# Kernel optimization log

Hardware: AMD Instinct MI355X
Metric: run time of the kernel (lower is better)

The kernel has to match this reference:

```python
import jax, jax.numpy as jnp
import numpy as np

N = 4096
D = 512
NC_RATIO = 0.1
GAMMA = 0.8
REG = 0.03
NITER = 100
THRESH = 1e-4


def setup_inputs() -> dict:
    key = jax.random.key(0)
    k1, k2, k3 = jax.random.split(key, 3)

    def unit(k):
        x = jax.random.normal(k, (N, D), dtype=jnp.float32)
        return x / jnp.linalg.norm(x, axis=1, keepdims=True)

    return {
        "image_embeds": unit(k1),
        "text_embeds": unit(k2),
        "text_no_embeds": unit(k3),
        "logit_scale": jnp.ones((), dtype=jnp.float32),
    }


def _sinkhorn_log(p, q, C, mask):
    """Log-domain Sinkhorn, faithful to sinkhorn_log_domain_torch (incl. early stop)."""
    logp, logq = jnp.log(p), jnp.log(q)

    def Mfun(u, v):
        Mm = (-C + u[:, None] + v[None, :]) / REG
        return jnp.where(mask == 0, jnp.float32(-1e6), Mm)

    def lse(A):  # log-sum-exp over axis 1, with the original +1e-10
        mx = jnp.max(A, axis=1, keepdims=True)
        return jnp.log(jnp.sum(jnp.exp(A - mx), axis=1) + 1e-10) + mx[:, 0]

    def cond(s):
        i, u, v, err = s
        return jnp.logical_and(i < NITER, err >= THRESH)

    def body(s):
        i, u, v, _ = s
        u1 = u
        u = REG * (logp - lse(Mfun(u, v))) + u
        v = REG * (logq - lse(Mfun(u, v).T)) + v
        return i + 1, u, v, jnp.sum(jnp.abs(u - u1))

    _, u, v, _ = jax.lax.while_loop(
        cond, body, (jnp.int32(0), 0.0 * p, 0.0 * q, jnp.float32(jnp.inf))
    )
    return jnp.exp(Mfun(u, v))


def _kl_batchmean(log_probs, target):
    # torch KLDivLoss(reduction='batchmean'): sum(t*(log t - lp)) / batch, t=0 -> 0
    pointwise = jnp.where(target > 0, target * jnp.log(target), 0.0) - target * log_probs
    return jnp.sum(pointwise) / target.shape[0]


def _forward(image_embeds, text_embeds, text_no_embeds, logit_scale):
    n = image_embeds.shape[0]
    scale = jnp.exp(logit_scale)
    sims = image_embeds @ text_embeds.T                        # [N, N]
    sims_no = jnp.sum(image_embeds * text_no_embeds, axis=1)[:, None]  # [N, 1]
    logits = jnp.concatenate([scale * sims, scale * sims_no], axis=1)  # [N, N+1]

    # ---- torch.no_grad() label construction ----
    sims_sg = jax.lax.stop_gradient(sims)
    sims_no_sg = jax.lax.stop_gradient(sims_no)
    scale_sg = jax.lax.stop_gradient(scale)

    # infoNCE_preds with temp = 1/scale
    pos = jnp.exp(jnp.diag(sims_sg) * scale_sg)
    neg_sum = jnp.sum(jnp.exp(sims_sg * scale_sg), axis=1) - pos
    preds = pos / (pos + neg_sum)
    nc_num = int(NC_RATIO * n)
    _, nc_ids = jax.lax.top_k(-preds, nc_num)  # smallest preds

    S = jnp.concatenate([sims_sg, sims_no_sg], axis=1)  # [N, N+1]
    cost_v = 1.0 - S
    cost_v = cost_v / jnp.max(cost_v)
    cost_t = 1.0 - S.T
    cost_t = cost_t / jnp.max(cost_t)
    p = jnp.full((n,), 1.0 / n, dtype=jnp.float32)
    q = jnp.full((n + 1,), 1.0 / (n + 1), dtype=jnp.float32)

    Mv = (jnp.ones((n, n + 1), dtype=jnp.int32)
          .at[:, -1].set(0)
          .at[nc_ids, nc_ids].set(0)
          .at[nc_ids, -1].set(1))

    pi_v = _sinkhorn_log(p, q, cost_v, Mv)
    pi_t = _sinkhorn_log(q, p, cost_t, Mv.T)

    idx = jnp.arange(n)
    Lv = (jnp.zeros((n, n + 1), dtype=jnp.float32)
          .at[idx, idx].set(1.0)
          .at[nc_ids, nc_ids].set(0.0)
          .at[nc_ids, -1].set(1.0))

    label_v2t = GAMMA * (pi_v / jnp.sum(pi_v, axis=1, keepdims=True)) + (1.0 - GAMMA) * Lv
    label_t2v = GAMMA * (pi_t / jnp.sum(pi_t, axis=1, keepdims=True)) + (1.0 - GAMMA) * Lv.T
    label_v2t = jax.lax.stop_gradient(label_v2t)
    label_t2v = jax.lax.stop_gradient(label_t2v)
    # ---- end no_grad ----

    loss_img = _kl_batchmean(jax.nn.log_softmax(logits, axis=1), label_v2t)
    loss_txt = _kl_batchmean(jax.nn.log_softmax(logits.T, axis=1), label_t2v)
    loss_ul = (loss_img + loss_txt) / 2.0

    cos = jnp.sum(text_embeds * text_no_embeds, axis=1)
    loss_op = jnp.mean(jnp.maximum(cos + 0.2, 0.0) + jnp.maximum(-0.7 - cos, 0.0))
    return loss_ul, loss_op


def reference(image_embeds, text_embeds, text_no_embeds, logit_scale):
    return _forward(image_embeds, text_embeds, text_no_embeds, logit_scale)
```

## Files before the change

kernel.cpp:

```cpp
#include <hip/hip_runtime.h>
#include <hip/hip_bf16.h>


#define NN 4096
#define LDA 4104
#define DD 512
#define NCNUM 409
#define REGc 0.03f
#define INVREG (1.0f/0.03f)
#define GAM 0.8f
#define THRESHc 1e-4f
#define LOGN 8.3177661667193433f
#define LOGM 8.3180102775477533f
#define NEGINF (-__builtin_inff())

typedef unsigned short u16;
typedef unsigned int u32;
typedef _Float16 f16;

struct alignas(16) Q  { u32 x, y, z, w; };
union H8 { Q q; f16 h[8]; };

typedef __attribute__((ext_vector_type(8))) short frag_ab;
typedef __attribute__((ext_vector_type(4))) float frag_cd;

__device__ __forceinline__ float bf2f(u32 u) { return __uint_as_float(u << 16); }
__device__ __forceinline__ float bflo(u32 w) { return __uint_as_float(w << 16); }
__device__ __forceinline__ float bfhi(u32 w) { return __uint_as_float(w & 0xFFFF0000u); }
__device__ __forceinline__ u16 f2bf_rne(float f) {
  u32 b = __float_as_uint(f);
  b += 0x7FFFu + ((b >> 16) & 1u);
  return (u16)(b >> 16);
}
__device__ __forceinline__ u16 f2h_hw(float f) {
  union { f16 h; u16 u; } X; X.h = (f16)f; return X.u;
}
__device__ __forceinline__ float h2f_hw(u16 v) {
  union { u16 u; f16 h; } X; X.u = v; return (float)X.h;
}
__device__ __forceinline__ float exp2_fast(float x) {
#if __has_builtin(__builtin_amdgcn_exp2f)
  return __builtin_amdgcn_exp2f(x);
#else
  float r; asm("v_exp_f32 %0, %1" : "=v"(r) : "v"(x)); return r;
#endif
}
__device__ __forceinline__ float ldu(const float* p) {
  return __hip_atomic_load(p, __ATOMIC_RELAXED, __HIP_MEMORY_SCOPE_AGENT);
}
__device__ __forceinline__ void stu(float* p, float v) {
  __hip_atomic_store(p, v, __ATOMIC_RELAXED, __HIP_MEMORY_SCOPE_AGENT);
}
__device__ __forceinline__ void gload_lds16(const u16* g, u16* l) {
  __builtin_amdgcn_global_load_lds(
      (const __attribute__((address_space(1))) u32*)g,
      (__attribute__((address_space(3))) u32*)l, 16, 0, 0);
}
__device__ __forceinline__ void unpack8(Q q, float* x) {
  H8 u; u.q = q;
  #pragma unroll
  for (int c = 0; c < 8; ++c) x[c] = (float)u.h[c];
}
__device__ __forceinline__ void lse_merge(float& m, float& s, float om, float os) {
  float nm = fmaxf(m, om);
  if (nm == NEGINF) return;
  float acc = 0.f;
  if (s  > 0.f) acc += s  * __expf(m  - nm);
  if (os > 0.f) acc += os * __expf(om - nm);
  m = nm; s = acc;
}
__device__ __forceinline__ float blockReduce256(float v) {
  __shared__ float sh[4];
  #pragma unroll
  for (int off = 32; off >= 1; off >>= 1) v += __shfl_xor(v, off);
  int w = threadIdx.x >> 6;
  if ((threadIdx.x & 63) == 0) sh[w] = v;
  __syncthreads();
  float r = 0.f;
  if (threadIdx.x == 0) r = sh[0] + sh[1] + sh[2] + sh[3];
  __syncthreads();
  return r;
}

__global__ void ContrastiveLoss_83391085019222_kernel(float* out) {
  if (threadIdx.x == 0) { out[0] = 0.5f; out[1] = 0.5f; }
}
__global__ void diag_kernel(float* out, float a, float b) {
  if (threadIdx.x == 0) { out[0] = a; out[1] = b; }
}

__global__ void detect_kernel(const u16* img, float* misc) {
  const int lane = threadIdx.x;
  float nb = 0.f, nf = 0.f;
  const float* fimg = (const float*)img;
  for (int c = lane * 8; c < lane * 8 + 8; ++c) {
    float xb = bf2f((u32)img[c]);
    nb += xb * xb;
    float xf = fimg[c];
    if (fabsf(xf) < 1e10f) nf += xf * xf; else nf += 1e10f;
  }
  #pragma unroll
  for (int off = 32; off >= 1; off >>= 1) { nb += __shfl_xor(nb, off); nf += __shfl_xor(nf, off); }
  if (lane == 0) {
    float db = fabsf(nb - 1.f);
    float df = fabsf(nf - 1.f);
    if (!(db == db)) db = 1e30f;
    if (!(df == df)) df = 1e30f;
    ((int*)misc)[10] = (df < db) ? 1 : 0;
  }
}

__global__ void cvt_kernel(const u16* img, const u16* txt,
                           u16* Abf, u16* Bbf, const float* misc) {
  const int isF = ((const int*)misc)[10];
  const int t = blockIdx.x * 256 + threadIdx.x;
  const int base = t * 4;
  if (isF) {
    const float* fi = (const float*)img;
    const float* ft = (const float*)txt;
    ushort4 oa, ob;
    oa.x = f2bf_rne(fi[base+0]); oa.y = f2bf_rne(fi[base+1]);
    oa.z = f2bf_rne(fi[base+2]); oa.w = f2bf_rne(fi[base+3]);
    ob.x = f2bf_rne(ft[base+0]); ob.y = f2bf_rne(ft[base+1]);
    ob.z = f2bf_rne(ft[base+2]); ob.w = f2bf_rne(ft[base+3]);
    *(ushort4*)(Abf + base) = oa;
    *(ushort4*)(Bbf + base) = ob;
  } else {
    *(ushort4*)(Abf + base) = *(const ushort4*)(img + base);
    *(ushort4*)(Bbf + base) = *(const ushort4*)(txt + base);
  }
}

__global__ void init_kernel(const u16* ls, float* vecs, float* errs,
                            float* rsA0, float* csA0, int* bar, float* misc) {
  int t = blockIdx.x * 256 + threadIdx.x;
  if (t < 16400) vecs[t] = 0.f;
  if (t < 256)  errs[t] = 0.f;
  if (t < 4096) rsA0[t] = 0.f;
  if (t < 4104) csA0[t] = 0.f;
  if (t < 1024) bar[t] = 0;
  if (t == 0) {
    const int isF = ((const int*)misc)[10];
    float lsv = isF ? ((const float*)ls)[0] : bf2f((u32)ls[0]);
    misc[0] = __expf(lsv);
  }
}

__global__ __launch_bounds__(256) void gemm_mfma(const u16* Abf, const u16* Bbf,
                                                 u16* S, float* gmin) {
  __shared__ float red[256];
  __shared__ u16 ldsA[128 * 64];
  __shared__ u16 ldsB[128 * 64];
  const int tid = threadIdx.x;
  const int wave = tid >> 6, lane = tid & 63;
  const int wr = wave >> 1, wc = wave & 1;
  const int rb = (int)blockIdx.y * 128;
  const int cb = (int)blockIdx.x * 128;
  const int l15 = lane & 15, q = lane >> 4;
  const int srow = lane >> 3;
  const int scol = (lane & 7) * 8;

  frag_cd acc[4][4];
  #pragma unroll
  for (int i = 0; i < 4; ++i)
    #pragma unroll
    for (int j = 0; j < 4; ++j) acc[i][j] = (frag_cd){0.f, 0.f, 0.f, 0.f};

  for (int kt = 0; kt < DD; kt += 64) {
    __syncthreads();
    #pragma unroll
    for (int i = 0; i < 4; ++i) {
      const int R = (wave * 4 + i) * 8;
      gload_lds16(Abf + (size_t)(rb + R + srow) * DD + kt + scol, &ldsA[R * 64]);
      gload_lds16(Bbf + (size_t)(cb + R + srow) * DD + kt + scol, &ldsB[R * 64]);
    }
    __syncthreads();
    #pragma unroll
    for (int s = 0; s < 2; ++s) {
      frag_ab af[4], bfr[4];
      #pragma unroll
      for (int t = 0; t < 4; ++t) {
        af[t]  = *(const frag_ab*)&ldsA[(wr * 64 + t * 16 + l15) * 64 + s * 32 + q * 8];
        bfr[t] = *(const frag_ab*)&ldsB[(wc * 64 + t * 16 + l15) * 64 + s * 32 + q * 8];
      }
      #pragma unroll
      for (int i = 0; i < 4; ++i)
        #pragma unroll
        for (int j = 0; j < 4; ++j)
          acc[i][j] = __builtin_amdgcn_mfma_f32_16x16x32_bf16(af[i], bfr[j], acc[i][j], 0, 0, 0);
    }
  }

  float lmin = 1e30f;
  #pragma unroll
  for (int i = 0; i < 4; ++i) {
    #pragma unroll
    for (int j = 0; j < 4; ++j) {
      #pragma unroll
      for (int r = 0; r < 4; ++r) {
        const int row = rb + wr * 64 + i * 16 + q * 4 + r;
        const int col = cb + wc * 64 + j * 16 + l15;
        u16 h = f2h_hw(acc[i][j][r]);
        lmin = fminf(lmin, h2f_hw(h));
        S[(size_t)row * LDA + col] = h;
      }
    }
  }
  red[tid] = lmin;
  __syncthreads();
  for (int sN = 128; sN >= 1; sN >>= 1) {
    if (tid < sN) red[tid] = fminf(red[tid], red[tid + sN]);
    __syncthreads();
  }
  if (tid == 0) gmin[blockIdx.y * 32 + blockIdx.x] = red[0];
}

__global__ void colvec_kernel(const u16* img, const u16* txt, const u16* tno,
                              u16* S, float* colvals, float* opP, const float* misc) {
  __shared__ float shOp[4];
  const int isF = ((const int*)misc)[10];
  const int wv = threadIdx.x >> 6;
  const int row = (int)(blockIdx.x << 2) + wv;
  const int lane = threadIdx.x & 63;
  const size_t base = (size_t)row * DD + lane * 8;
  float xi[8], xt[8], xn[8];
  if (isF) {
    const float* fi = (const float*)img;
    const float* ft = (const float*)txt;
    const float* fn = (const float*)tno;
    #pragma unroll
    for (int c = 0; c < 8; ++c) { xi[c] = fi[base+c]; xt[c] = ft[base+c]; xn[c] = fn[base+c]; }
  } else {
    Q qi = *(const Q*)(img + base);
    Q qt = *(const Q*)(txt + base);
    Q qn = *(const Q*)(tno + base);
    xi[0]=bflo(qi.x); xi[1]=bfhi(qi.x); xi[2]=bflo(qi.y); xi[3]=bfhi(qi.y);
    xi[4]=bflo(qi.z); xi[5]=bfhi(qi.z); xi[6]=bflo(qi.w); xi[7]=bfhi(qi.w);
    xt[0]=bflo(qt.x); xt[1]=bfhi(qt.x); xt[2]=bflo(qt.y); xt[3]=bfhi(qt.y);
    xt[4]=bflo(qt.z); xt[5]=bfhi(qt.z); xt[6]=bflo(qt.w); xt[7]=bfhi(qt.w);
    xn[0]=bflo(qn.x); xn[1]=bfhi(qn.x); xn[2]=bflo(qn.y); xn[3]=bfhi(qn.y);
    xn[4]=bflo(qn.z); xn[5]=bfhi(qn.z); xn[6]=bflo(qn.w); xn[7]=bfhi(qn.w);
  }
  float sn = 0.f, cs = 0.f;
  #pragma unroll
  for (int c = 0; c < 8; ++c) { sn += xi[c]*xn[c]; cs += xt[c]*xn[c]; }
  #pragma unroll
  for (int off = 32; off >= 1; off >>= 1) { sn += __shfl_xor(sn, off); cs += __shfl_xor(cs, off); }
  if (lane == 0) {
    colvals[row] = sn;
    S[(size_t)row * LDA + NN] = f2h_hw(sn);
    shOp[wv] = fmaxf(cs + 0.2f, 0.f) + fmaxf(-0.7f - cs, 0.f);
  }
  __syncthreads();
  if (threadIdx.x == 0) opP[blockIdx.x] = shOp[0] + shOp[1] + shOp[2] + shOp[3];
}

__global__ void reduce_kernel(const float* gmin, const float* colvals,
                              const float* opP, float* misc) {
  __shared__ float smin[256];
  __shared__ float ssum[256];
  float mn = 1e30f, sm = 0.f;
  for (int i = threadIdx.x; i < 1024; i += 256) mn = fminf(mn, gmin[i]);
  for (int i = threadIdx.x; i < 4096; i += 256) mn = fminf(mn, h2f_hw(f2h_hw(colvals[i])));
  for (int i = threadIdx.x; i < 1024; i += 256) sm += opP[i];
  smin[threadIdx.x] = mn; ssum[threadIdx.x] = sm;
  __syncthreads();
  for (int sN = 128; sN >= 1; sN >>= 1) {
    if (threadIdx.x < sN) {
      smin[threadIdx.x] = fminf(smin[threadIdx.x], smin[threadIdx.x + sN]);
      ssum[threadIdx.x] += ssum[threadIdx.x + sN];
    }
    __syncthreads();
  }
  if (threadIdx.x == 0) {
    float maxC = 1.0f - smin[0];
    float a = 1.0f / (maxC * REGc);
    misc[1] = a;
    misc[4] = ssum[0];
    misc[5] = __expf(-a);
    misc[6] = a * 1.4426950408889634f;
  }
}

__global__ void preds_kernel(const u16* S, const float* misc, float* preds) {
  const int row = (int)(blockIdx.x << 2) + (int)(threadIdx.x >> 6);
  const int lane = threadIdx.x & 63;
  const float scale = misc[0];
  const u16* Sr = S + (size_t)row * LDA;
  float m = NEGINF, s = 0.f;
  for (int it = 0; it < 8; ++it) {
    const int j0 = (it << 9) + (lane << 3);
    float x[8];
    unpack8(*(const Q*)(Sr + j0), x);
    float lm = NEGINF;
    #pragma unroll
    for (int c = 0; c < 8; ++c) { x[c] *= scale; lm = fmaxf(lm, x[c]); }
    float lsum = 0.f;
    #pragma unroll
    for (int c = 0; c < 8; ++c) lsum += __expf(x[c] - lm);
    lse_merge(m, s, lm, lsum);
  }
  #pragma unroll
  for (int off = 32; off >= 1; off >>= 1) {
    float om = __shfl_xor(m, off), os = __shfl_xor(s, off);
    lse_merge(m, s, om, os);
  }
  if (lane == 0) {
    float sii = h2f_hw(Sr[row]);
    preds[row] = __expf(scale * sii - m) / s;
  }
}

__global__ void rank_kernel(const float* preds, int* is_nc) {
  const int i = blockIdx.x;
  const float pv = preds[i];
  float cnt = 0.f;
  for (int k2 = threadIdx.x; k2 < NN; k2 += 256) {
    float pk = preds[k2];
    cnt += (pk < pv || (pk == pv && k2 < i)) ? 1.f : 0.f;
  }
  cnt = blockReduce256(cnt);
  if (threadIdx.x == 0) is_nc[i] = (cnt < (float)NCNUM) ? 1 : 0;
}

__device__ __forceinline__ bool unmasked(int j, int r, bool ncr) {
  return (j == NN) ? ncr : !((j == r) && ncr);
}

__device__ __forceinline__ void gridbar(int* bar, int bid, int phase, bool& dead) {
  __syncthreads();
  if (threadIdx.x == 0 && !dead) {
    const int g = bid & 31;
    if (__hip_atomic_fetch_add(&bar[g << 4], 1, __ATOMIC_RELAXED,
                               __HIP_MEMORY_SCOPE_AGENT) == 32 * phase - 1) {
      if (__hip_atomic_fetch_add(&bar[32 << 4], 1, __ATOMIC_RELAXED,
                                 __HIP_MEMORY_SCOPE_AGENT) == 32 * phase - 1) {
        #pragma unroll
        for (int gg = 0; gg < 32; ++gg)
          __hip_atomic_store(&bar[(gg << 4) + 8], phase, __ATOMIC_RELAXED,
                             __HIP_MEMORY_SCOPE_AGENT);
      }
    }
    int spins = 0;
    while (__hip_atomic_load(&bar[(g << 4) + 8], __ATOMIC_RELAXED,
                             __HIP_MEMORY_SCOPE_AGENT) < phase) {
      __builtin_amdgcn_s_sleep(2);
      if (++spins > (1 << 21)) { dead = true; break; }
    }
  }
  __syncthreads();
}

template<int RB, int FIN>
__device__ __forceinline__ void substep(
    float (&Ec)[8][8], int k,
    int c1, int c2, int c1p, int c2p,
    const float* prevRow, const float* prevCol,
    float* outRow, float* outCol,
    float* z1, float* z2, int nz1, int nz2,
    float* errs1, float* errs2,
    float* uvec, float* utvec, float* vvec, float* vtvec,
    float* shW1, float* shW2, float (*shAcc)[128], float* sh4096,
    float* se,
    float ea, int rt, int ct, int bid, int tid, int tc, int tr,
    int j0c, int r0, int cbase, bool isLast) {

  const int gRow = RB ? c2 : c1;
  const int gCol = RB ? c1 : c2;

  if (!FIN) {
    const int z = bid * 256 + tid;
    if (z < nz1) stu(&z1[z], 0.f);
    else if (z - nz1 < nz2) stu(&z2[z - nz1], 0.f);
  }

  float pr = 0.f, prN = 0.f;
  if (tid < 128) {
    pr = ldu(&prevRow[r0 + tid]);
  } else {
    pr = ldu(&prevCol[cbase + (tid - 128)]);
    if (isLast && tid == 128) prN = ldu(&prevCol[NN]);
  }

  float errd = 0.f;
  if (tid < 128) {
    const int i = r0 + tid;
    float w = 0.f;
    if (!RB) {
      if (!FIN && !gCol) w = (k == 0) ? ea : ea / (4096.0f * pr);
      if (ct == 0 && k >= 1 && !c2p) vtvec[i] = REGc * (-LOGN - __logf(pr));
    } else {
      if (!gCol) {
        w = ea / (4096.0f * pr);
        if (ct == 0) {
          float un = REGc * (-LOGN - __logf(pr));
          errd = fabsf(un - uvec[i]);
          uvec[i] = un;
        }
      }
    }
    shW2[tid] = w;
  } else {
    const int j = cbase + (tid - 128);
    float w = 0.f;
    if (!RB) {
      if (!FIN && !gRow) w = (k == 0) ? ea : ea / (4097.0f * pr);
      if (rt == 0 && k >= 1 && !c1p) vvec[j] = REGc * (-LOGM - __logf(pr));
    } else {
      if (!gRow) {
        w = ea / (4097.0f * pr);
        if (rt == 0) {
          float un = REGc * (-LOGM - __logf(pr));
          errd = fabsf(un - utvec[j]);
          utvec[j] = un;
        }
      }
    }
    shW1[tid - 128] = w;
    if (isLast && tid == 128) {
      float w2 = 0.f;
      if (!RB) {
        if (!FIN && !gRow) w2 = (k == 0) ? ea : ea / (4097.0f * prN);
        if (rt == 0 && k >= 1 && !c1p) vvec[NN] = REGc * (-LOGM - __logf(prN));
      } else {
        if (!gRow) {
          w2 = ea / (4097.0f * prN);
          if (rt == 0) {
            float un = REGc * (-LOGM - __logf(prN));
            errd += fabsf(un - utvec[NN]);
            utvec[NN] = un;
          }
        }
      }
      shW1[128] = w2;
    }
  }
  __syncthreads();

  if (!FIN && !(gRow && gCol)) {
    float W1l[8];
    #pragma unroll
    for (int c = 0; c < 8; ++c) W1l[c] = shW1[j0c + c];
    float cs[8];
    #pragma unroll
    for (int c = 0; c < 8; ++c) cs[c] = 0.f;
    const float w4096 = isLast ? shW1[128] : 0.f;
    #pragma unroll
    for (int st = 0; st < 8; ++st) {
      const int rr = (st << 4) + tr;
      if (!gCol) {
        const float Wr = shW2[rr];
        #pragma unroll
        for (int c = 0; c < 8; ++c) cs[c] = fmaf(Ec[st][c], Wr, cs[c]);
      }
      if (!gRow) {
        float rs = 0.f;
        #pragma unroll
        for (int c = 0; c < 8; ++c) rs = fmaf(Ec[st][c], W1l[c], rs);
        #pragma unroll
        for (int off = 8; off >= 1; off >>= 1) rs += __shfl_xor(rs, off);
        if (tc == 0) {
          if (isLast) rs += sh4096[rr] * w4096;
          atomicAdd(&outRow[r0 + rr], rs);
        }
      }
    }
    if (!gCol) {
      #pragma unroll
      for (int c = 0; c < 8; ++c) shAcc[tr][j0c + c] = cs[c];
      __syncthreads();
      if (tid < 128) {
        float s2 = 0.f;
        #pragma unroll
        for (int g = 0; g < 16; ++g) s2 += shAcc[g][tid];
        atomicAdd(&outCol[cbase + tid], s2);
      }
      if (isLast && tid >= 128 && tid < 192) {
        const int l = tid - 128;
        float s3 = sh4096[l] * shW2[l] + sh4096[l + 64] * shW2[l + 64];
        #pragma unroll
        for (int off = 32; off >= 1; off >>= 1) s3 += __shfl_xor(s3, off);
        if (l == 0) atomicAdd(&outCol[NN], s3);
      }
    }
  }

  if (RB) {
    float e2 = errd;
    #pragma unroll
    for (int off = 32; off >= 1; off >>= 1) e2 += __shfl_xor(e2, off);
    if ((tid & 63) == 0) se[tid >> 6] = e2;
    __syncthreads();
    if (tid == 0) {
      if (ct == 0) atomicAdd(&errs1[k], se[0] + se[1]);
      if (rt == 0) atomicAdd(&errs2[k], se[2] + se[3]);
    }
  }
}

__global__ __launch_bounds__(256, 4) void sink_persist(
    const u16* S, const float* misc, float* errs1, float* errs2,
    float* uvec, float* utvec, float* vvec, float* vtvec,
    float* rsA0, float* rsA1, float* csA0, float* csA1,
    float* rsB0, float* rsB1, float* csB0, float* csB1,
    const int* is_nc, int* bar) {
  __shared__ float shW1[129];
  __shared__ float shW2[128];
  __shared__ float shAcc[16][128];
  __shared__ float sh4096[128];
  __shared__ int   shG[4];
  __shared__ float se[4];

  const int tid = threadIdx.x;
  const int rt = blockIdx.x, ct = blockIdx.y;
  const int bid = ct * 32 + rt;
  const int cbase = ct << 7, r0 = rt << 7;
  const float a = misc[1], ea = misc[5], b = misc[6];
  const int tc = tid & 15, tr = tid >> 4;
  const int j0c = tc << 3;
  const bool isLast = (ct == 31);

  float Ec[8][8];
  if (rt != ct) {
    #pragma unroll
    for (int st = 0; st < 8; ++st) {
      const int rr = (st << 4) + tr;
      H8 hh; hh.q = *(const Q*)(S + (size_t)(r0 + rr) * LDA + cbase + j0c);
      #pragma unroll
      for (int c = 0; c < 8; ++c) Ec[st][c] = exp2_fast((float)hh.h[c] * b);
    }
  } else {
    #pragma unroll
    for (int st = 0; st < 8; ++st) {
      const int rr = (st << 4) + tr;
      const int r = r0 + rr;
      float xv[8];
      unpack8(*(const Q*)(S + (size_t)r * LDA + cbase + j0c), xv);
      const bool ncr = (is_nc[r] != 0);
      #pragma unroll
      for (int c = 0; c < 8; ++c) {
        float e = __expf(xv[c] * a);
        if ((j0c + c == rr) && ncr) e = 0.f;
        Ec[st][c] = e;
      }
    }
  }
  if (isLast && tid < 128) {
    const int r = r0 + tid;
    float x = h2f_hw(S[(size_t)r * LDA + NN]);
    sh4096[tid] = (is_nc[r] != 0) ? __expf(x * a) : 0.f;
  }
  __syncthreads();

  bool dead = false;
  int phase = 0;
  for (int k = 0; k < 100; ++k) {
    const int p = k & 1;
    const int q2 = 1 - p;
    const int pm = (k > 0) ? q2 : 0;
    if (tid < 4) {
      const int kk = k - 1 - (tid >> 1);
      const float* ep = (tid & 1) ? errs2 : errs1;
      shG[tid] = (kk >= 0) && (ldu(&ep[kk]) < THRESHc);
    }
    __syncthreads();
    const int c1 = shG[0], c2 = shG[1], c1p = shG[2], c2p = shG[3];
    if (c1 && c2 && c1p && c2p) break;

    substep<0, 0>(Ec, k, c1, c2, c1p, c2p,
        pm ? rsB1 : rsB0, pm ? csB1 : csB0,
        p ? rsA1 : rsA0, p ? csA1 : csA0,
        p ? csB1 : csB0, p ? rsB1 : rsB0, 4104, 4096,
        errs1, errs2, uvec, utvec, vvec, vtvec,
        shW1, shW2, shAcc, sh4096, se,
        ea, rt, ct, bid, tid, tc, tr, j0c, r0, cbase, isLast);
    gridbar(bar, bid, ++phase, dead);

    substep<1, 0>(Ec, k, c1, c2, c1p, c2p,
        p ? rsA1 : rsA0, p ? csA1 : csA0,
        p ? rsB1 : rsB0, p ? csB1 : csB0,
        q2 ? rsA1 : rsA0, q2 ? csA1 : csA0, 4096, 4104,
        errs1, errs2, uvec, utvec, vvec, vtvec,
        shW1, shW2, shAcc, sh4096, se,
        ea, rt, ct, bid, tid, tc, tr, j0c, r0, cbase, isLast);
    gridbar(bar, bid, ++phase, dead);
  }

  if (tid < 4) {
    const int kk = 99 - (tid >> 1);
    const float* ep = (tid & 1) ? errs2 : errs1;
    shG[tid] = (ldu(&ep[kk]) < THRESHc);
  }
  __syncthreads();
  substep<0, 1>(Ec, 100, shG[0], shG[1], shG[2], shG[3],
      rsB1, csB1, rsA0, csA0, rsA0, csA0, 0, 0,
      errs1, errs2, uvec, utvec, vvec, vtvec,
      shW1, shW2, shAcc, sh4096, se,
      ea, rt, ct, bid, tid, tc, tr, j0c, r0, cbase, isLast);
}

__global__ __launch_bounds__(256) void final_pass(const u16* S, const float* vvec,
                           const float* vtvec, const float* misc, const int* is_nc,
                           float* rowLm, float* rowLs, float* rowGs,
                           float* colLm, float* colLs, float* colGs) {
  const float a = misc[1], scale = misc[0];
  const int ct = blockIdx.x, rt = blockIdx.y;
  const int tid = threadIdx.x;
  const int tc = tid & 15, tr = tid >> 4;
  const int cbase = ct << 7, r0 = rt << 7;
  const int j0 = cbase + (tc << 3);
  const bool anyv = (j0 <= NN);
  float wc[8]; unsigned jval = 0;
  #pragma unroll
  for (int c = 0; c < 8; ++c) {
    int j = j0 + c;
    wc[c] = 0.f;
    if (j <= NN) { jval |= 1u << c; wc[c] = vvec[j] * INVREG; }
  }
  float cLm[8], cLs[8], cGs[8];
  #pragma unroll
  for (int c = 0; c < 8; ++c) { cLm[c] = NEGINF; cLs[c] = 0.f; cGs[c] = 0.f; }
  for (int st = 0; st < 8; ++st) {
    const int r = r0 + (st << 4) + tr;
    float xv[8], lg[8]; unsigned um = 0;
    #pragma unroll
    for (int c = 0; c < 8; ++c) { xv[c] = 0.f; lg[c] = 0.f; }
    if (anyv) {
      float raw[8];
      unpack8(*(const Q*)(S + (size_t)r * LDA + j0), raw);
      const bool ncr = (is_nc[r] != 0);
      const float vtr = vtvec[r] * INVREG;
      #pragma unroll
      for (int c = 0; c < 8; ++c) {
        if (!(jval >> c & 1u)) continue;
        xv[c] = raw[c] * a;
        lg[c] = scale * raw[c];
        cGs[c] += __expf(lg[c]);
        if (unmasked(j0 + c, r, ncr)) {
          um |= 1u << c;
          float e2 = xv[c] + vtr;
          float nm = fmaxf(cLm[c], e2);
          cLs[c] = cLs[c] * __expf(cLm[c] - nm) + __expf(e2 - nm);
          cLm[c] = nm;
        }
      }
    }
    float rsG = 0.f;
    if (anyv) {
      #pragma unroll
      for (int c = 0; c < 8; ++c) if (jval >> c & 1u) rsG += __expf(lg[c]);
    }
    #pragma unroll
    for (int off = 8; off >= 1; off >>= 1) rsG += __shfl_xor(rsG, off);
    float rmL = NEGINF;
    if (anyv) {
      #pragma unroll
      for (int c = 0; c < 8; ++c) if (um >> c & 1u) rmL = fmaxf(rmL, xv[c] + wc[c]);
    }
    #pragma unroll
    for (int off = 8; off >= 1; off >>= 1) rmL = fmaxf(rmL, __shfl_xor(rmL, off));
    float rsL = 0.f;
    if (anyv && rmL > NEGINF) {
      #pragma unroll
      for (int c = 0; c < 8; ++c) if (um >> c & 1u) rsL += __expf(xv[c] + wc[c] - rmL);
    }
    #pragma unroll
    for (int off = 8; off >= 1; off >>= 1) rsL += __shfl_xor(rsL, off);
    if (tc == 0) {
      rowGs[ct * NN + r] = rsG;
      rowLm[ct * NN + r] = rmL;
      rowLs[ct * NN + r] = rsL;
    }
  }
  __shared__ float shm[16][128];
  __shared__ float shs[16][128];
  #pragma unroll
  for (int c = 0; c < 8; ++c) { shm[tr][(tc << 3) + c] = cLm[c]; shs[tr][(tc << 3) + c] = cLs[c]; }
  __syncthreads();
  if (tid < 128) {
    float m = NEGINF, s = 0.f;
    #pragma unroll
    for (int g = 0; g < 16; ++g) lse_merge(m, s, shm[g][tid], shs[g][tid]);
    const int j = cbase + tid;
    if (j <= NN) { colLm[rt * LDA + j] = m; colLs[rt * LDA + j] = s; }
  }
  __syncthreads();
  #pragma unroll
  for (int c = 0; c < 8; ++c) shs[tr][(tc << 3) + c] = cGs[c];
  __syncthreads();
  if (tid < 128) {
    float s = 0.f;
    #pragma unroll
    for (int g = 0; g < 16; ++g) s += shs[g][tid];
    const int j = cbase + tid;
    if (j <= NN) colGs[rt * LDA + j] = s;
  }
}

__global__ void final_combine(const float* rowLm, const float* rowLs, const float* rowGs,
                              const float* colLm, const float* colLs, const float* colGs,
                              float* LSMrow, float* LBLm, float* LBLs,
                              float* LSMcol, float* LBTm, float* LBTs) {
  const int b = blockIdx.x;
  if (b < 16) {
    const int i = (b << 8) + threadIdx.x;
    float m = NEGINF, s = 0.f, sg = 0.f;
    for (int t = 0; t < 33; ++t) {
      lse_merge(m, s, rowLm[t * NN + i], rowLs[t * NN + i]);
      sg += rowGs[t * NN + i];
    }
    LBLm[i] = m; LBLs[i] = s;
    LSMrow[i] = __logf(sg);
  } else {
    const int j = ((b - 16) << 8) + threadIdx.x;
    if (j <= NN) {
      float m = NEGINF, s = 0.f, sg = 0.f;
      for (int t = 0; t < 32; ++t) {
        lse_merge(m, s, colLm[t * LDA + j], colLs[t * LDA + j]);
        sg += colGs[t * LDA + j];
      }
      LBTm[j] = m; LBTs[j] = s;
      LSMcol[j] = __logf(sg);
    }
  }
}

__global__ __launch_bounds__(256) void loss_pass(const u16* S, const float* vvec,
                          const float* vtvec, const float* misc, const int* is_nc,
                          const float* LSMrow, const float* LBLm, const float* LBLs,
                          const float* LSMcol, const float* LBTm, const float* LBTs,
                          float* imgP, float* txtP) {
  const float a = misc[1], scale = misc[0];
  const int ct = blockIdx.x, rt = blockIdx.y;
  const int tid = threadIdx.x;
  const int tc = tid & 15, tr = tid >> 4;
  const int cbase = ct << 7, r0 = rt << 7;
  const int j0 = cbase + (tc << 3);
  const bool anyv = (j0 <= NN);
  float vcw[8], bm[8], bsi[8], cg[8]; unsigned jval = 0;
  #pragma unroll
  for (int c = 0; c < 8; ++c) {
    int j = j0 + c;
    vcw[c] = 0.f; bm[c] = 0.f; bsi[c] = 0.f; cg[c] = 0.f;
    if (j <= NN) {
      jval |= 1u << c;
      vcw[c] = vvec[j] * INVREG; bm[c] = LBTm[j]; bsi[c] = 1.f / LBTs[j]; cg[c] = LSMcol[j];
    }
  }
  float sImg = 0.f, sTxt = 0.f;
  for (int st = 0; st < 8; ++st) {
    const int r = r0 + (st << 4) + tr;
    if (anyv) {
      float raw[8];
      unpack8(*(const Q*)(S + (size_t)r * LDA + j0), raw);
      const bool ncr = (is_nc[r] != 0);
      const float vtr = vtvec[r] * INVREG;
      const float rm = LBLm[r], rsi = 1.f / LBLs[r], rg = LSMrow[r];
      #pragma unroll
      for (int c = 0; c < 8; ++c) {
        if (!(jval >> c & 1u)) continue;
        const int j = j0 + c;
        float xv = raw[c] * a;
        float lgt = scale * raw[c];
        bool unm = unmasked(j, r, ncr);
        bool lv = (j == NN) ? ncr : ((j == r) && !ncr);
        float rr = unm ? __expf(xv + vcw[c] - rm) * rsi : 0.f;
        float t = GAM * rr + (lv ? 0.2f : 0.f);
        if (t > 0.f) sImg += t * (__logf(t) - (lgt - rg));
        float r2 = unm ? __expf(xv + vtr - bm[c]) * bsi[c] : 0.f;
        float t2 = GAM * r2 + (lv ? 0.2f : 0.f);
        if (t2 > 0.f) sTxt += t2 * (__logf(t2) - (lgt - cg[c]));
      }
    }
  }
  sImg = blockReduce256(sImg);
  sTxt = blockReduce256(sTxt);
  if (tid == 0) { imgP[rt * 33 + ct] = sImg; txtP[rt * 33 + ct] = sTxt; }
}

__global__ void finish_kernel(const float* imgP, const float* txtP,
                              const float* misc, float* out) {
  float vi = 0.f, vtx = 0.f;
  for (int idx = threadIdx.x; idx < 1056; idx += 256) { vi += imgP[idx]; vtx += txtP[idx]; }
  vi = blockReduce256(vi);
  vtx = blockReduce256(vtx);
  if (threadIdx.x == 0) {
    float loss_img = vi / 4096.0f;
    float loss_txt = vtx / 4097.0f;
    float loss_ul = 0.5f * (loss_img + loss_txt);
    float loss_op = misc[4] / 4096.0f;
    if (vi == 0.f && vtx == 0.f) loss_ul = 777.0f;
    if (!(loss_ul == loss_ul))   loss_ul = 888.0f;
    out[0] = loss_ul;
    out[1] = loss_op;
  }
}

extern "C" void kernel_launch(void* const* d_in, const int* in_sizes, int n_in,
                              void* d_out, int out_size, void* d_ws, size_t ws_size,
                              hipStream_t stream) {
  (void)in_sizes; (void)n_in; (void)out_size;
  const u16* img = (const u16*)d_in[0];
  const u16* txt = (const u16*)d_in[1];
  const u16* tno = (const u16*)d_in[2];
  const u16* ls  = (const u16*)d_in[3];
  float* out = (float*)d_out;

  ContrastiveLoss_83391085019222_kernel<<<1, 64, 0, stream>>>(out);

  size_t off = 0;
  char* w = (char*)d_ws;
  u16* S; u16* Abf; u16* Bbf;
  float *rsA0, *rsA1, *csA0, *csA1, *rsB0, *rsB1, *csB0, *csB1, *errs;
  float *rowLm, *rowLs, *rowGs, *colLm, *colLs, *colGs;
  float *vecs, *preds, *colvals, *gmin, *opP;
  float *LSMrow, *LBLm, *LBLs, *LSMcol, *LBTm, *LBTs, *imgP, *txtP, *misc;
  int* is_nc; int* bar;
  #define ALLOC(ptr, type, nbytes) ptr = (type)(w + off); off = (off + (size_t)(nbytes) + 255) & ~(size_t)255
  ALLOC(S,      u16*,   (size_t)NN * LDA * 2);
  ALLOC(Abf,    u16*,   (size_t)NN * DD * 2);
  ALLOC(Bbf,    u16*,   (size_t)NN * DD * 2);
  ALLOC(rsA0,   float*, 4096 * 4);
  ALLOC(rsA1,   float*, 4096 * 4);
  ALLOC(csA0,   float*, 4104 * 4);
  ALLOC(csA1,   float*, 4104 * 4);
  ALLOC(rsB0,   float*, 4096 * 4);
  ALLOC(rsB1,   float*, 4096 * 4);
  ALLOC(csB0,   float*, 4104 * 4);
  ALLOC(csB1,   float*, 4104 * 4);
  ALLOC(errs,   float*, 256 * 4);
  ALLOC(rowLm,  float*, (size_t)33 * NN * 4);
  ALLOC(rowLs,  float*, (size_t)33 * NN * 4);
  ALLOC(rowGs,  float*, (size_t)33 * NN * 4);
  ALLOC(colLm,  float*, (size_t)32 * LDA * 4);
  ALLOC(colLs,  float*, (size_t)32 * LDA * 4);
  ALLOC(colGs,  float*, (size_t)32 * LDA * 4);
  ALLOC(vecs,   float*, 16400 * 4);
  ALLOC(preds,  float*, NN * 4);
  ALLOC(is_nc,  int*,   NN * 4);
  ALLOC(colvals,float*, NN * 4);
  ALLOC(gmin,   float*, 1024 * 4);
  ALLOC(opP,    float*, 1024 * 4);
  ALLOC(LSMrow, float*, NN * 4);
  ALLOC(LBLm,   float*, NN * 4);
  ALLOC(LBLs,   float*, NN * 4);
  ALLOC(LSMcol, float*, LDA * 4);
  ALLOC(LBTm,   float*, LDA * 4);
  ALLOC(LBTs,   float*, LDA * 4);
  ALLOC(imgP,   float*, 1056 * 4);
  ALLOC(txtP,   float*, 1056 * 4);
  ALLOC(bar,    int*,   4096);
  ALLOC(misc,   float*, 64);
  #undef ALLOC

  if (ws_size < off) {
    diag_kernel<<<1, 64, 0, stream>>>(out, -(float)(ws_size / 1000000.0),
                                      -(float)(off / 1000000.0));
    return;
  }

  float* uvec  = vecs;
  float* vvec  = vecs + 4096;
  float* utvec = vecs + 8200;
  float* vtvec = vecs + 12304;
  float* errs1 = errs;
  float* errs2 = errs + 128;

  detect_kernel<<<1, 64, 0, stream>>>(img, misc);
  cvt_kernel<<<2048, 256, 0, stream>>>(img, txt, Abf, Bbf, misc);
  init_kernel<<<65, 256, 0, stream>>>(ls, vecs, errs, rsA0, csA0, bar, misc);
  gemm_mfma<<<dim3(32, 32), 256, 0, stream>>>(Abf, Bbf, S, gmin);
  colvec_kernel<<<1024, 256, 0, stream>>>(img, txt, tno, S, colvals, opP, misc);
  reduce_kernel<<<1, 256, 0, stream>>>(gmin, colvals, opP, misc);

  preds_kernel<<<1024, 256, 0, stream>>>(S, misc, preds);
  rank_kernel<<<4096, 256, 0, stream>>>(preds, is_nc);

  sink_persist<<<dim3(32, 32), 256, 0, stream>>>(S, misc, errs1, errs2,
      uvec, utvec, vvec, vtvec,
      rsA0, rsA1, csA0, csA1, rsB0, rsB1, csB0, csB1,
      is_nc, bar);

  final_pass<<<dim3(33, 32), 256, 0, stream>>>(S, vvec, vtvec, misc, is_nc,
                                               rowLm, rowLs, rowGs, colLm, colLs, colGs);
  final_combine<<<33, 256, 0, stream>>>(rowLm, rowLs, rowGs, colLm, colLs, colGs,
                                        LSMrow, LBLm, LBLs, LSMcol, LBTm, LBTs);
  loss_pass<<<dim3(33, 32), 256, 0, stream>>>(S, vvec, vtvec, misc, is_nc,
                                              LSMrow, LBLm, LBLs, LSMcol, LBTm, LBTs, imgP, txtP);
  finish_kernel<<<1, 256, 0, stream>>>(imgP, txtP, misc, out);
}
```

Before: 347.1 us.

## Fuse final, combine, loss and finish passes into persistent Sinkhorn kernel

Folds the post-Sinkhorn final_pass, final_combine, loss_pass and finish_kernel into the persistent sink_persist kernel, separated by grid barriers, so four kernel launches and their S reloads into fresh blocks are removed. The extra 4097th column that used to need a 33rd block column is handled by the last column-tile blocks. Prev-row/col loads are hoisted out of substep into the loop before the shG sync, and stores switch to uncached stu/ldu so data is visible across the grid. In exchange it adds several grid barriers, extra shared memory that may lower occupancy of the persistent kernel, and serial work on a single block for the final reduction.

```diff
diff --git a/kernel.cpp b/kernel.cpp
--- a/kernel.cpp
+++ b/kernel.cpp
@@ -355,7 +355,7 @@
 __device__ __forceinline__ void substep(
     float (&Ec)[8][8], int k,
     int c1, int c2, int c1p, int c2p,
-    const float* prevRow, const float* prevCol,
+    float pr, float prN,
     float* outRow, float* outCol,
     float* z1, float* z2, int nz1, int nz2,
     float* errs1, float* errs2,
@@ -374,21 +374,13 @@
     else if (z - nz1 < nz2) stu(&z2[z - nz1], 0.f);
   }
 
-  float pr = 0.f, prN = 0.f;
-  if (tid < 128) {
-    pr = ldu(&prevRow[r0 + tid]);
-  } else {
-    pr = ldu(&prevCol[cbase + (tid - 128)]);
-    if (isLast && tid == 128) prN = ldu(&prevCol[NN]);
-  }
-
   float errd = 0.f;
   if (tid < 128) {
     const int i = r0 + tid;
     float w = 0.f;
     if (!RB) {
       if (!FIN && !gCol) w = (k == 0) ? ea : ea / (4096.0f * pr);
-      if (ct == 0 && k >= 1 && !c2p) vtvec[i] = REGc * (-LOGN - __logf(pr));
+      if (ct == 0 && k >= 1 && !c2p) stu(&vtvec[i], REGc * (-LOGN - __logf(pr)));
     } else {
       if (!gCol) {
         w = ea / (4096.0f * pr);
@@ -405,7 +397,7 @@
     float w = 0.f;
     if (!RB) {
       if (!FIN && !gRow) w = (k == 0) ? ea : ea / (4097.0f * pr);
-      if (rt == 0 && k >= 1 && !c1p) vvec[j] = REGc * (-LOGM - __logf(pr));
+      if (rt == 0 && k >= 1 && !c1p) stu(&vvec[j], REGc * (-LOGM - __logf(pr)));
     } else {
       if (!gRow) {
         w = ea / (4097.0f * pr);
@@ -421,7 +413,7 @@
       float w2 = 0.f;
       if (!RB) {
         if (!FIN && !gRow) w2 = (k == 0) ? ea : ea / (4097.0f * prN);
-        if (rt == 0 && k >= 1 && !c1p) vvec[NN] = REGc * (-LOGM - __logf(prN));
+        if (rt == 0 && k >= 1 && !c1p) stu(&vvec[NN], REGc * (-LOGM - __logf(prN)));
       } else {
         if (!gRow) {
           w2 = ea / (4097.0f * prN);
@@ -503,13 +495,20 @@
     float* uvec, float* utvec, float* vvec, float* vtvec,
     float* rsA0, float* rsA1, float* csA0, float* csA1,
     float* rsB0, float* rsB1, float* csB0, float* csB1,
-    const int* is_nc, int* bar) {
+    const int* is_nc, int* bar,
+    float* rowLm, float* rowLs, float* rowGs,
+    float* colLm, float* colLs, float* colGs,
+    float* LSMrow, float* LBLm, float* LBLs,
+    float* LSMcol, float* LBTm, float* LBTs,
+    float* imgP, float* txtP, float* out) {
   __shared__ float shW1[129];
   __shared__ float shW2[128];
   __shared__ float shAcc[16][128];
   __shared__ float sh4096[128];
   __shared__ int   shG[4];
   __shared__ float se[4];
+  __shared__ float shm[16][128];
+  __shared__ float shs[16][128];
 
   const int tid = threadIdx.x;
   const int rt = blockIdx.x, ct = blockIdx.y;
@@ -558,6 +557,15 @@
     const int p = k & 1;
     const int q2 = 1 - p;
     const int pm = (k > 0) ? q2 : 0;
+    const float* pRowA = pm ? rsB1 : rsB0;
+    const float* pColA = pm ? csB1 : csB0;
+    float prA = 0.f, prAN = 0.f;
+    if (tid < 128) {
+      prA = ldu(&pRowA[r0 + tid]);
+    } else {
+      prA = ldu(&pColA[cbase + (tid - 128)]);
+      if (isLast && tid == 128) prAN = ldu(&pColA[NN]);
+    }
     if (tid < 4) {
       const int kk = k - 1 - (tid >> 1);
       const float* ep = (tid & 1) ? errs2 : errs1;
@@ -567,8 +575,7 @@
     const int c1 = shG[0], c2 = shG[1], c1p = shG[2], c2p = shG[3];
     if (c1 && c2 && c1p && c2p) break;
 
-    substep<0, 0>(Ec, k, c1, c2, c1p, c2p,
-        pm ? rsB1 : rsB0, pm ? csB1 : csB0,
+    substep<0, 0>(Ec, k, c1, c2, c1p, c2p, prA, prAN,
         p ? rsA1 : rsA0, p ? csA1 : csA0,
         p ? csB1 : csB0, p ? rsB1 : rsB0, 4104, 4096,
         errs1, errs2, uvec, utvec, vvec, vtvec,
@@ -576,8 +583,16 @@
         ea, rt, ct, bid, tid, tc, tr, j0c, r0, cbase, isLast);
     gridbar(bar, bid, ++phase, dead);
 
-    substep<1, 0>(Ec, k, c1, c2, c1p, c2p,
-        p ? rsA1 : rsA0, p ? csA1 : csA0,
+    const float* pRowB = p ? rsA1 : rsA0;
+    const float* pColB = p ? csA1 : csA0;
+    float prB = 0.f, prBN = 0.f;
+    if (tid < 128) {
+      prB = ldu(&pRowB[r0 + tid]);
+    } else {
+      prB = ldu(&pColB[cbase + (tid - 128)]);
+      if (isLast && tid == 128) prBN = ldu(&pColB[NN]);
+    }
+    substep<1, 0>(Ec, k, c1, c2, c1p, c2p, prB, prBN,
         p ? rsB1 : rsB0, p ? csB1 : csB0,
         q2 ? rsA1 : rsA0, q2 ? csA1 : csA0, 4096, 4104,
         errs1, errs2, uvec, utvec, vvec, vtvec,
@@ -586,57 +601,50 @@
     gridbar(bar, bid, ++phase, dead);
   }
 
-  if (tid < 4) {
-    const int kk = 99 - (tid >> 1);
-    const float* ep = (tid & 1) ? errs2 : errs1;
-    shG[tid] = (ldu(&ep[kk]) < THRESHc);
-  }
-  __syncthreads();
-  substep<0, 1>(Ec, 100, shG[0], shG[1], shG[2], shG[3],
-      rsB1, csB1, rsA0, csA0, rsA0, csA0, 0, 0,
-      errs1, errs2, uvec, utvec, vvec, vtvec,
-      shW1, shW2, shAcc, sh4096, se,
-      ea, rt, ct, bid, tid, tc, tr, j0c, r0, cbase, isLast);
-}
-
-__global__ __launch_bounds__(256) void final_pass(const u16* S, const float* vvec,
-                           const float* vtvec, const float* misc, const int* is_nc,
-                           float* rowLm, float* rowLs, float* rowGs,
-                           float* colLm, float* colLs, float* colGs) {
-  const float a = misc[1], scale = misc[0];
-  const int ct = blockIdx.x, rt = blockIdx.y;
-  const int tid = threadIdx.x;
-  const int tc = tid & 15, tr = tid >> 4;
-  const int cbase = ct << 7, r0 = rt << 7;
-  const int j0 = cbase + (tc << 3);
-  const bool anyv = (j0 <= NN);
-  float wc[8]; unsigned jval = 0;
-  #pragma unroll
-  for (int c = 0; c < 8; ++c) {
-    int j = j0 + c;
-    wc[c] = 0.f;
-    if (j <= NN) { jval |= 1u << c; wc[c] = vvec[j] * INVREG; }
-  }
-  float cLm[8], cLs[8], cGs[8];
-  #pragma unroll
-  for (int c = 0; c < 8; ++c) { cLm[c] = NEGINF; cLs[c] = 0.f; cGs[c] = 0.f; }
-  for (int st = 0; st < 8; ++st) {
-    const int r = r0 + (st << 4) + tr;
-    float xv[8], lg[8]; unsigned um = 0;
-    #pragma unroll
-    for (int c = 0; c < 8; ++c) { xv[c] = 0.f; lg[c] = 0.f; }
-    if (anyv) {
+  {
+    float prF = 0.f, prFN = 0.f;
+    if (tid < 128) {
+      prF = ldu(&rsB1[r0 + tid]);
+    } else {
+      prF = ldu(&csB1[cbase + (tid - 128)]);
+      if (isLast && tid == 128) prFN = ldu(&csB1[NN]);
+    }
+    if (tid < 4) {
+      const int kk = 99 - (tid >> 1);
+      const float* ep = (tid & 1) ? errs2 : errs1;
+      shG[tid] = (ldu(&ep[kk]) < THRESHc);
+    }
+    __syncthreads();
+    substep<0, 1>(Ec, 100, shG[0], shG[1], shG[2], shG[3], prF, prFN,
+        rsA0, csA0, rsA0, csA0, 0, 0,
+        errs1, errs2, uvec, utvec, vvec, vtvec,
+        shW1, shW2, shAcc, sh4096, se,
+        ea, rt, ct, bid, tid, tc, tr, j0c, r0, cbase, isLast);
+  }
+
+  gridbar(bar, bid, ++phase, dead);
+  const float scale = misc[0];
+
+  {
+    float wc[8];
+    #pragma unroll
+    for (int c = 0; c < 8; ++c) wc[c] = ldu(&vvec[cbase + j0c + c]) * INVREG;
+    float cLm[8], cLs[8], cGs[8];
+    #pragma unroll
+    for (int c = 0; c < 8; ++c) { cLm[c] = NEGINF; cLs[c] = 0.f; cGs[c] = 0.f; }
+    for (int st = 0; st < 8; ++st) {
+      const int r = r0 + (st << 4) + tr;
+      float xv[8], lg[8]; unsigned um = 0;
       float raw[8];
-      unpack8(*(const Q*)(S + (size_t)r * LDA + j0), raw);
+      unpack8(*(const Q*)(S + (size_t)r * LDA + cbase + j0c), raw);
       const bool ncr = (is_nc[r] != 0);
-      const float vtr = vtvec[r] * INVREG;
+      const float vtr = ldu(&vtvec[r]) * INVREG;
       #pragma unroll
       for (int c = 0; c < 8; ++c) {
-        if (!(jval >> c & 1u)) continue;
         xv[c] = raw[c] * a;
         lg[c] = scale * raw[c];
         cGs[c] += __expf(lg[c]);
-        if (unmasked(j0 + c, r, ncr)) {
+        if (!((cbase + j0c + c == r) && ncr)) {
           um |= 1u << c;
           float e2 = xv[c] + vtr;
           float nm = fmaxf(cLm[c], e2);
@@ -644,155 +652,217 @@
           cLm[c] = nm;
         }
       }
-    }
-    float rsG = 0.f;
-    if (anyv) {
-      #pragma unroll
-      for (int c = 0; c < 8; ++c) if (jval >> c & 1u) rsG += __expf(lg[c]);
-    }
-    #pragma unroll
-    for (int off = 8; off >= 1; off >>= 1) rsG += __shfl_xor(rsG, off);
-    float rmL = NEGINF;
-    if (anyv) {
+      float rsG = 0.f;
+      #pragma unroll
+      for (int c = 0; c < 8; ++c) rsG += __expf(lg[c]);
+      #pragma unroll
+      for (int off = 8; off >= 1; off >>= 1) rsG += __shfl_xor(rsG, off);
+      float rmL = NEGINF;
       #pragma unroll
       for (int c = 0; c < 8; ++c) if (um >> c & 1u) rmL = fmaxf(rmL, xv[c] + wc[c]);
-    }
-    #pragma unroll
-    for (int off = 8; off >= 1; off >>= 1) rmL = fmaxf(rmL, __shfl_xor(rmL, off));
-    float rsL = 0.f;
-    if (anyv && rmL > NEGINF) {
-      #pragma unroll
-      for (int c = 0; c < 8; ++c) if (um >> c & 1u) rsL += __expf(xv[c] + wc[c] - rmL);
-    }
-    #pragma unroll
-    for (int off = 8; off >= 1; off >>= 1) rsL += __shfl_xor(rsL, off);
-    if (tc == 0) {
-      rowGs[ct * NN + r] = rsG;
-      rowLm[ct * NN + r] = rmL;
-      rowLs[ct * NN + r] = rsL;
-    }
-  }
-  __shared__ float shm[16][128];
-  __shared__ float shs[16][128];
-  #pragma unroll
-  for (int c = 0; c < 8; ++c) { shm[tr][(tc << 3) + c] = cLm[c]; shs[tr][(tc << 3) + c] = cLs[c]; }
-  __syncthreads();
-  if (tid < 128) {
-    float m = NEGINF, s = 0.f;
-    #pragma unroll
-    for (int g = 0; g < 16; ++g) lse_merge(m, s, shm[g][tid], shs[g][tid]);
-    const int j = cbase + tid;
-    if (j <= NN) { colLm[rt * LDA + j] = m; colLs[rt * LDA + j] = s; }
-  }
-  __syncthreads();
-  #pragma unroll
-  for (int c = 0; c < 8; ++c) shs[tr][(tc << 3) + c] = cGs[c];
-  __syncthreads();
-  if (tid < 128) {
-    float s = 0.f;
-    #pragma unroll
-    for (int g = 0; g < 16; ++g) s += shs[g][tid];
-    const int j = cbase + tid;
-    if (j <= NN) colGs[rt * LDA + j] = s;
-  }
-}
-
-__global__ void final_combine(const float* rowLm, const float* rowLs, const float* rowGs,
-                              const float* colLm, const float* colLs, const float* colGs,
-                              float* LSMrow, float* LBLm, float* LBLs,
-                              float* LSMcol, float* LBTm, float* LBTs) {
-  const int b = blockIdx.x;
-  if (b < 16) {
-    const int i = (b << 8) + threadIdx.x;
-    float m = NEGINF, s = 0.f, sg = 0.f;
-    for (int t = 0; t < 33; ++t) {
-      lse_merge(m, s, rowLm[t * NN + i], rowLs[t * NN + i]);
-      sg += rowGs[t * NN + i];
-    }
-    LBLm[i] = m; LBLs[i] = s;
-    LSMrow[i] = __logf(sg);
-  } else {
-    const int j = ((b - 16) << 8) + threadIdx.x;
-    if (j <= NN) {
-      float m = NEGINF, s = 0.f, sg = 0.f;
-      for (int t = 0; t < 32; ++t) {
-        lse_merge(m, s, colLm[t * LDA + j], colLs[t * LDA + j]);
-        sg += colGs[t * LDA + j];
-      }
-      LBTm[j] = m; LBTs[j] = s;
-      LSMcol[j] = __logf(sg);
-    }
-  }
-}
-
-__global__ __launch_bounds__(256) void loss_pass(const u16* S, const float* vvec,
-                          const float* vtvec, const float* misc, const int* is_nc,
-                          const float* LSMrow, const float* LBLm, const float* LBLs,
-                          const float* LSMcol, const float* LBTm, const float* LBTs,
-                          float* imgP, float* txtP) {
-  const float a = misc[1], scale = misc[0];
-  const int ct = blockIdx.x, rt = blockIdx.y;
-  const int tid = threadIdx.x;
-  const int tc = tid & 15, tr = tid >> 4;
-  const int cbase = ct << 7, r0 = rt << 7;
-  const int j0 = cbase + (tc << 3);
-  const bool anyv = (j0 <= NN);
-  float vcw[8], bm[8], bsi[8], cg[8]; unsigned jval = 0;
-  #pragma unroll
-  for (int c = 0; c < 8; ++c) {
-    int j = j0 + c;
-    vcw[c] = 0.f; bm[c] = 0.f; bsi[c] = 0.f; cg[c] = 0.f;
-    if (j <= NN) {
-      jval |= 1u << c;
-      vcw[c] = vvec[j] * INVREG; bm[c] = LBTm[j]; bsi[c] = 1.f / LBTs[j]; cg[c] = LSMcol[j];
-    }
-  }
-  float sImg = 0.f, sTxt = 0.f;
-  for (int st = 0; st < 8; ++st) {
-    const int r = r0 + (st << 4) + tr;
-    if (anyv) {
+      #pragma unroll
+      for (int off = 8; off >= 1; off >>= 1) rmL = fmaxf(rmL, __shfl_xor(rmL, off));
+      float rsL = 0.f;
+      if (rmL > NEGINF) {
+        #pragma unroll
+        for (int c = 0; c < 8; ++c) if (um >> c & 1u) rsL += __expf(xv[c] + wc[c] - rmL);
+      }
+      #pragma unroll
+      for (int off = 8; off >= 1; off >>= 1) rsL += __shfl_xor(rsL, off);
+      if (tc == 0) {
+        stu(&rowGs[ct * NN + r], rsG);
+        stu(&rowLm[ct * NN + r], rmL);
+        stu(&rowLs[ct * NN + r], rsL);
+      }
+    }
+    #pragma unroll
+    for (int c = 0; c < 8; ++c) { shm[tr][j0c + c] = cLm[c]; shs[tr][j0c + c] = cLs[c]; }
+    __syncthreads();
+    if (tid < 128) {
+      float m = NEGINF, s = 0.f;
+      #pragma unroll
+      for (int g = 0; g < 16; ++g) lse_merge(m, s, shm[g][tid], shs[g][tid]);
+      stu(&colLm[rt * LDA + cbase + tid], m);
+      stu(&colLs[rt * LDA + cbase + tid], s);
+    }
+    __syncthreads();
+    #pragma unroll
+    for (int c = 0; c < 8; ++c) shs[tr][j0c + c] = cGs[c];
+    __syncthreads();
+    if (tid < 128) {
+      float s = 0.f;
+      #pragma unroll
+      for (int g = 0; g < 16; ++g) s += shs[g][tid];
+      stu(&colGs[rt * LDA + cbase + tid], s);
+    }
+    if (isLast) {
+      __syncthreads();
+      if (tid < 128) {
+        const int r = r0 + tid;
+        float rawN = h2f_hw(S[(size_t)r * LDA + NN]);
+        int ncrN = is_nc[r];
+        float rsG = __expf(scale * rawN);
+        float xvN = rawN * a;
+        float wcN = ldu(&vvec[NN]) * INVREG;
+        float rmL = ncrN ? (xvN + wcN) : NEGINF;
+        float rsL = ncrN ? 1.f : 0.f;
+        stu(&rowGs[32 * NN + r], rsG);
+        stu(&rowLm[32 * NN + r], rmL);
+        stu(&rowLs[32 * NN + r], rsL);
+      }
+      float cLmN = NEGINF, cLsN = 0.f, cGsN = 0.f;
+      if (tc == 0) {
+        #pragma unroll
+        for (int st = 0; st < 8; ++st) {
+          const int r = r0 + (st << 4) + tr;
+          float rw = h2f_hw(S[(size_t)r * LDA + NN]);
+          float xvN = rw * a;
+          cGsN += __expf(scale * rw);
+          if (is_nc[r]) {
+            float vtr = ldu(&vtvec[r]) * INVREG;
+            float e2 = xvN + vtr;
+            float nm = fmaxf(cLmN, e2);
+            cLsN = cLsN * __expf(cLmN - nm) + __expf(e2 - nm);
+            cLmN = nm;
+          }
+        }
+      }
+      __syncthreads();
+      if (tc == 0) { shm[tr][0] = cLmN; shs[tr][0] = cLsN; shAcc[tr][0] = cGsN; }
+      __syncthreads();
+      if (tid == 0) {
+        float m = NEGINF, s = 0.f, sg = 0.f;
+        for (int g = 0; g < 16; ++g) {
+          lse_merge(m, s, shm[g][0], shs[g][0]);
+          sg += shAcc[g][0];
+        }
+        stu(&colLm[rt * LDA + NN], m);
+        stu(&colLs[rt * LDA + NN], s);
+        stu(&colGs[rt * LDA + NN], sg);
+      }
+    }
+  }
+  gridbar(bar, bid, ++phase, dead);
+
+  {
+    int o = bid * 8 + tid;
+    bool act = (tid < 8);
+    if (bid == 1023 && tid == 8) { act = true; o = 8192; }
+    if (act) {
+      if (o < 4096) {
+        const int i = o;
+        float m = NEGINF, s = 0.f, sg = 0.f;
+        for (int t = 0; t < 33; ++t) {
+          lse_merge(m, s, ldu(&rowLm[t * NN + i]), ldu(&rowLs[t * NN + i]));
+          sg += ldu(&rowGs[t * NN + i]);
+        }
+        stu(&LBLm[i], m); stu(&LBLs[i], s);
+        stu(&LSMrow[i], __logf(sg));
+      } else {
+        const int j = o - 4096;
+        float m = NEGINF, s = 0.f, sg = 0.f;
+        for (int t = 0; t < 32; ++t) {
+          lse_merge(m, s, ldu(&colLm[t * LDA + j]), ldu(&colLs[t * LDA + j]));
+          sg += ldu(&colGs[t * LDA + j]);
+        }
+        stu(&LBTm[j], m); stu(&LBTs[j], s);
+        stu(&LSMcol[j], __logf(sg));
+      }
+    }
+  }
+  gridbar(bar, bid, ++phase, dead);
+
+  {
+    float vcw[8], bm[8], bsi[8], cg[8];
+    #pragma unroll
+    for (int c = 0; c < 8; ++c) {
+      const int j = cbase + j0c + c;
+      vcw[c] = ldu(&vvec[j]) * INVREG;
+      bm[c] = ldu(&LBTm[j]);
+      bsi[c] = 1.f / ldu(&LBTs[j]);
+      cg[c] = ldu(&LSMcol[j]);
+    }
+    float sImg = 0.f, sTxt = 0.f;
+    for (int st = 0; st < 8; ++st) {
+      const int r = r0 + (st << 4) + tr;
       float raw[8];
-      unpack8(*(const Q*)(S + (size_t)r * LDA + j0), raw);
+      unpack8(*(const Q*)(S + (size_t)r * LDA + cbase + j0c), raw);
       const bool ncr = (is_nc[r] != 0);
-      const float vtr = vtvec[r] * INVREG;
-      const float rm = LBLm[r], rsi = 1.f / LBLs[r], rg = LSMrow[r];
+      const float vtr = ldu(&vtvec[r]) * INVREG;
+      const float rm = ldu(&LBLm[r]), rsi = 1.f / ldu(&LBLs[r]), rg = ldu(&LSMrow[r]);
       #pragma unroll
       for (int c = 0; c < 8; ++c) {
-        if (!(jval >> c & 1u)) continue;
-        const int j = j0 + c;
+        const int j = cbase + j0c + c;
         float xv = raw[c] * a;
         float lgt = scale * raw[c];
-        bool unm = unmasked(j, r, ncr);
-        bool lv = (j == NN) ? ncr : ((j == r) && !ncr);
-        float rr = unm ? __expf(xv + vcw[c] - rm) * rsi : 0.f;
-        float t = GAM * rr + (lv ? 0.2f : 0.f);
+        bool unm = !((j == r) && ncr);
+        bool lv = (j == r) && !ncr;
+        float rr2 = unm ? __expf(xv + vcw[c] - rm) * rsi : 0.f;
+        float t = GAM * rr2 + (lv ? 0.2f : 0.f);
         if (t > 0.f) sImg += t * (__logf(t) - (lgt - rg));
         float r2 = unm ? __expf(xv + vtr - bm[c]) * bsi[c] : 0.f;
         float t2 = GAM * r2 + (lv ? 0.2f : 0.f);
         if (t2 > 0.f) sTxt += t2 * (__logf(t2) - (lgt - cg[c]));
       }
     }
-  }
-  sImg = blockReduce256(sImg);
-  sTxt = blockReduce256(sTxt);
-  if (tid == 0) { imgP[rt * 33 + ct] = sImg; txtP[rt * 33 + ct] = sTxt; }
-}
-
-__global__ void finish_kernel(const float* imgP, const float* txtP,
-                              const float* misc, float* out) {
-  float vi = 0.f, vtx = 0.f;
-  for (int idx = threadIdx.x; idx < 1056; idx += 256) { vi += imgP[idx]; vtx += txtP[idx]; }
-  vi = blockReduce256(vi);
-  vtx = blockReduce256(vtx);
-  if (threadIdx.x == 0) {
-    float loss_img = vi / 4096.0f;
-    float loss_txt = vtx / 4097.0f;
-    float loss_ul = 0.5f * (loss_img + loss_txt);
-    float loss_op = misc[4] / 4096.0f;
-    if (vi == 0.f && vtx == 0.f) loss_ul = 777.0f;
-    if (!(loss_ul == loss_ul))   loss_ul = 888.0f;
-    out[0] = loss_ul;
-    out[1] = loss_op;
+    sImg = blockReduce256(sImg);
+    sTxt = blockReduce256(sTxt);
+    if (tid == 0) {
+      stu(&imgP[rt * 33 + ct], sImg);
+      stu(&txtP[rt * 33 + ct], sTxt);
+    }
+    if (isLast) {
+      float sI = 0.f, sT = 0.f;
+      if (tc == 0) {
+        const float vcwN = ldu(&vvec[NN]) * INVREG;
+        const float bmN = ldu(&LBTm[NN]);
+        const float bsiN = 1.f / ldu(&LBTs[NN]);
+        const float cgN = ldu(&LSMcol[NN]);
+        #pragma unroll
+        for (int st = 0; st < 8; ++st) {
+          const int r = r0 + (st << 4) + tr;
+          float rw = h2f_hw(S[(size_t)r * LDA + NN]);
+          const bool ncr = (is_nc[r] != 0);
+          float xv = rw * a;
+          float lgt = scale * rw;
+          const float vtr = ldu(&vtvec[r]) * INVREG;
+          const float rm = ldu(&LBLm[r]), rsi = 1.f / ldu(&LBLs[r]), rg = ldu(&LSMrow[r]);
+          float rr2 = ncr ? __expf(xv + vcwN - rm) * rsi : 0.f;
+          float t = GAM * rr2 + (ncr ? 0.2f : 0.f);
+          if (t > 0.f) sI += t * (__logf(t) - (lgt - rg));
+          float r2 = ncr ? __expf(xv + vtr - bmN) * bsiN : 0.f;
+          float t2 = GAM * r2 + (ncr ? 0.2f : 0.f);
+          if (t2 > 0.f) sT += t2 * (__logf(t2) - (lgt - cgN));
+        }
+      }
+      sI = blockReduce256(sI);
+      sT = blockReduce256(sT);
+      if (tid == 0) {
+        stu(&imgP[rt * 33 + 32], sI);
+        stu(&txtP[rt * 33 + 32], sT);
+      }
+    }
+  }
+  gridbar(bar, bid, ++phase, dead);
+
+  if (bid == 0) {
+    float vi = 0.f, vtx = 0.f;
+    for (int idx = tid; idx < 1056; idx += 256) {
+      vi += ldu(&imgP[idx]);
+      vtx += ldu(&txtP[idx]);
+    }
+    vi = blockReduce256(vi);
+    vtx = blockReduce256(vtx);
+    if (tid == 0) {
+      float loss_img = vi / 4096.0f;
+      float loss_txt = vtx / 4097.0f;
+      float loss_ul = 0.5f * (loss_img + loss_txt);
+      float loss_op = misc[4] / 4096.0f;
+      if (vi == 0.f && vtx == 0.f) loss_ul = 777.0f;
+      if (!(loss_ul == loss_ul))   loss_ul = 888.0f;
+      out[0] = loss_ul;
+      out[1] = loss_op;
+    }
   }
 }
 
@@ -879,13 +949,8 @@
   sink_persist<<<dim3(32, 32), 256, 0, stream>>>(S, misc, errs1, errs2,
       uvec, utvec, vvec, vtvec,
       rsA0, rsA1, csA0, csA1, rsB0, rsB1, csB0, csB1,
-      is_nc, bar);
-
-  final_pass<<<dim3(33, 32), 256, 0, stream>>>(S, vvec, vtvec, misc, is_nc,
-                                               rowLm, rowLs, rowGs, colLm, colLs, colGs);
-  final_combine<<<33, 256, 0, stream>>>(rowLm, rowLs, rowGs, colLm, colLs, colGs,
-                                        LSMrow, LBLm, LBLs, LSMcol, LBTm, LBTs);
-  loss_pass<<<dim3(33, 32), 256, 0, stream>>>(S, vvec, vtvec, misc, is_nc,
-                                              LSMrow, LBLm, LBLs, LSMcol, LBTm, LBTs, imgP, txtP);
-  finish_kernel<<<1, 256, 0, stream>>>(imgP, txtP, misc, out);
-}
+      is_nc, bar,
+      rowLm, rowLs, rowGs, colLm, colLs, colGs,
+      LSMrow, LBLm, LBLs, LSMcol, LBTm, LBTs,
+      imgP, txtP, out);
+}
```

Result: no change. 340.7 us (-1.8%).
